# Performance work log

Hardware: AMD Instinct MI355X
Metric: run time of the kernel (lower is better)

Reference implementation:

```python
import jax, jax.numpy as jnp
import numpy as np

HEADS = 16
DIM_HEAD = 64
QUERY_DIM = 1024


def setup_inputs() -> dict:
    key = jax.random.key(0)
    ks = jax.random.split(key, 5)
    B, S, D = 4, 2048, QUERY_DIM
    inner = HEADS * DIM_HEAD
    s = 0.02
    return {
        "x": jax.random.normal(ks[0], (B, S, D), dtype=jnp.float32),
        "Wq": jax.random.normal(ks[1], (D, inner), dtype=jnp.float32) * s,
        "Wk": jax.random.normal(ks[2], (D, inner), dtype=jnp.float32) * s,
        "Wv": jax.random.normal(ks[3], (D, inner), dtype=jnp.float32) * s,
        "Wo": jax.random.normal(ks[4], (inner, D), dtype=jnp.float32) * s,
    }


def reference(x, Wq, Wk, Wv, Wo):
    B, S, D = x.shape
    h, d = HEADS, DIM_HEAD
    scale = d ** (-0.5)
    # projections -> [B, h, S, d]
    q = (x @ Wq).reshape(B, S, h, d).transpose(0, 2, 1, 3)
    k = (x @ Wk).reshape(B, S, h, d).transpose(0, 2, 1, 3)
    v = (x @ Wv).reshape(B, S, h, d).transpose(0, 2, 1, 3)
    # scores [B, h, S, S]
    attn = jnp.einsum("bhqd,bhkd->bhqk", q, k) * scale
    attn = jax.nn.softmax(attn, axis=-1)
    out = jnp.einsum("bhqk,bhkd->bhqd", attn, v)
    out = out.transpose(0, 2, 1, 3).reshape(B, S, h * d)
    return out @ Wo
```

## Files before the change

kernel.cpp:

```cpp
#include <hip/hip_runtime.h>
#include <cstddef>

#define BATCH  4
#define SLEN   2048
#define NHEADS 16
#define DHEAD  64
#define DMODEL 1024

typedef __attribute__((ext_vector_type(8)))  short short8;
typedef __attribute__((ext_vector_type(4)))  float f32x4;
typedef __attribute__((ext_vector_type(16))) float f32x16;

__device__ inline unsigned short f2bf(float f) {
    union { float f; unsigned int u; } v; v.f = f;
    unsigned int r = v.u + 0x7fffu + ((v.u >> 16) & 1u);
    return (unsigned short)(r >> 16);
}

__device__ inline float fast_exp2(float x) {
#if __has_builtin(__builtin_amdgcn_exp2f)
    return __builtin_amdgcn_exp2f(x);
#else
    return __expf(x * 0.69314718f);
#endif
}

__device__ inline void gload_lds16(const unsigned short* g, unsigned short* l) {
    __builtin_amdgcn_global_load_lds(
        (const __attribute__((address_space(1))) void*)g,
        (__attribute__((address_space(3))) void*)l, 16, 0, 0);
}

__global__ __launch_bounds__(256)
void convert_bf16(const float* __restrict__ src, unsigned short* __restrict__ dst, int n8)
{
    const int i = blockIdx.x * 256 + threadIdx.x;
    if (i >= n8) return;
    const float4 a = ((const float4*)src)[2 * i];
    const float4 b = ((const float4*)src)[2 * i + 1];
    short8 o;
    o[0] = (short)f2bf(a.x); o[1] = (short)f2bf(a.y);
    o[2] = (short)f2bf(a.z); o[3] = (short)f2bf(a.w);
    o[4] = (short)f2bf(b.x); o[5] = (short)f2bf(b.y);
    o[6] = (short)f2bf(b.z); o[7] = (short)f2bf(b.w);
    ((short8*)dst)[i] = o;
}

__global__ __launch_bounds__(256)
void wtrans(const float* __restrict__ W0, const float* __restrict__ W1,
            const float* __restrict__ W2, const float* __restrict__ W3,
            unsigned short* __restrict__ T0, unsigned short* __restrict__ T1,
            unsigned short* __restrict__ T2, unsigned short* __restrict__ T3)
{
    const int z = blockIdx.z;
    const float* W = (z == 0) ? W0 : (z == 1) ? W1 : (z == 2) ? W2 : W3;
    unsigned short* Wt = (z == 0) ? T0 : (z == 1) ? T1 : (z == 2) ? T2 : T3;

    __shared__ unsigned short T[64 * 72];
    const int tid = threadIdx.x;
    const int n0 = blockIdx.x * 64, k0 = blockIdx.y * 64;

    #pragma unroll
    for (int it = 0; it < 2; it++) {
        const int t2 = it * 256 + tid;
        const int row = t2 >> 3, col8 = (t2 & 7) * 8;
        const float4 a = *(const float4*)(W + (size_t)(k0 + row) * DMODEL + n0 + col8);
        const float4 b = *(const float4*)(W + (size_t)(k0 + row) * DMODEL + n0 + col8 + 4);
        short8 o;
        o[0] = (short)f2bf(a.x); o[1] = (short)f2bf(a.y);
        o[2] = (short)f2bf(a.z); o[3] = (short)f2bf(a.w);
        o[4] = (short)f2bf(b.x); o[5] = (short)f2bf(b.y);
        o[6] = (short)f2bf(b.z); o[7] = (short)f2bf(b.w);
        *(short8*)&T[row * 72 + col8] = o;
    }
    __syncthreads();
    #pragma unroll
    for (int it = 0; it < 2; it++) {
        const int t2 = it * 256 + tid;
        const int nn = t2 >> 3, k8 = (t2 & 7) * 8;
        short8 v;
        #pragma unroll
        for (int j = 0; j < 8; j++) v[j] = (short)T[(k8 + j) * 72 + nn];
        *(short8*)(Wt + (size_t)(n0 + nn) * DMODEL + k0 + k8) = v;
    }
}

template<int KIND>
__global__ __launch_bounds__(256)
void gemm_bf16(const unsigned short* __restrict__ A,
               const unsigned short* __restrict__ B0,
               const unsigned short* __restrict__ B1,
               const unsigned short* __restrict__ B2,
               void* __restrict__ C0v, void* __restrict__ C1v, void* __restrict__ C2v)
{
    constexpr int N = DMODEL, K = DMODEL;
    __shared__ unsigned short As[128 * 64];
    __shared__ unsigned short Bs[128 * 64];

    const int z = blockIdx.z;
    const unsigned short* Bw = (z == 0) ? B0 : (z == 1) ? B1 : B2;
    void* Cv = (z == 0) ? C0v : (z == 1) ? C1v : C2v;

    const int tid  = threadIdx.x;
    const int lane = tid & 63;
    const int wave = tid >> 6;
    const int c  = lane & 15, qd = lane >> 4;
    const int wr = wave >> 1, wc = wave & 1;
    const int m0 = blockIdx.y * 128, n0 = blockIdx.x * 128;

    const unsigned short* ag[4];
    const unsigned short* bg[4];
    unsigned short* al[4];
    unsigned short* bl[4];
    #pragma unroll
    for (int j = 0; j < 4; j++) {
        const int cid = j * 256 + tid;
        const int row = cid >> 3;
        const int k8  = (cid & 7) ^ (row & 7);
        ag[j] = A  + (size_t)(m0 + row) * K + k8 * 8;
        bg[j] = Bw + (size_t)(n0 + row) * K + k8 * 8;
        al[j] = &As[cid * 8];
        bl[j] = &Bs[cid * 8];
    }

    f32x4 acc[4][4];
    #pragma unroll
    for (int mb = 0; mb < 4; mb++)
        #pragma unroll
        for (int nb = 0; nb < 4; nb++)
            #pragma unroll
            for (int r = 0; r < 4; r++) acc[mb][nb][r] = 0.f;

    for (int k0 = 0; k0 < K; k0 += 64) {
        __syncthreads();
        #pragma unroll
        for (int j = 0; j < 4; j++) {
            gload_lds16(ag[j], al[j]);
            gload_lds16(bg[j], bl[j]);
            ag[j] += 64; bg[j] += 64;
        }
        __syncthreads();

        #pragma unroll
        for (int ks = 0; ks < 2; ks++) {
            const int sw = (ks * 4 + qd) ^ (c & 7);
            short8 af[4], bf[4];
            #pragma unroll
            for (int mb = 0; mb < 4; mb++)
                af[mb] = *(const short8*)&As[((wr * 64 + mb * 16 + c) * 8 + sw) * 8];
            #pragma unroll
            for (int nb = 0; nb < 4; nb++)
                bf[nb] = *(const short8*)&Bs[((wc * 64 + nb * 16 + c) * 8 + sw) * 8];
            #pragma unroll
            for (int mb = 0; mb < 4; mb++)
                #pragma unroll
                for (int nb = 0; nb < 4; nb++)
                    acc[mb][nb] = __builtin_amdgcn_mfma_f32_16x16x32_bf16(
                        af[mb], bf[nb], acc[mb][nb], 0, 0, 0);
        }
    }

    const int mbase = m0 + wr * 64 + qd * 4;
    const int nbase = n0 + wc * 64 + c;
    if (KIND == 1) {
        float* C = (float*)Cv;
        #pragma unroll
        for (int mb = 0; mb < 4; mb++)
            #pragma unroll
            for (int nb = 0; nb < 4; nb++)
                #pragma unroll
                for (int r = 0; r < 4; r++)
                    C[(size_t)(mbase + mb * 16 + r) * N + nbase + nb * 16] = acc[mb][nb][r];
    } else if (z != 2) {
        unsigned short* C = (unsigned short*)Cv;
        const float osc = (z == 0) ? 0.18033688f : 1.0f;
        #pragma unroll
        for (int mb = 0; mb < 4; mb++)
            #pragma unroll
            for (int nb = 0; nb < 4; nb++)
                #pragma unroll
                for (int r = 0; r < 4; r++)
                    C[(size_t)(mbase + mb * 16 + r) * N + nbase + nb * 16] =
                        f2bf(acc[mb][nb][r] * osc);
    } else {
        unsigned short* C = (unsigned short*)Cv;
        const int b = mbase >> 11;
        #pragma unroll
        for (int mb = 0; mb < 4; mb++) {
            const int s = (mbase + mb * 16) & 2047;
            #pragma unroll
            for (int nb = 0; nb < 4; nb++) {
                const int n = nbase + nb * 16;
                const int h = n >> 6, dd = n & 63;
                ushort4 val = make_ushort4(f2bf(acc[mb][nb][0]), f2bf(acc[mb][nb][1]),
                                           f2bf(acc[mb][nb][2]), f2bf(acc[mb][nb][3]));
                *(ushort4*)(C + ((size_t)((b * 16 + h) * 64 + dd)) * SLEN + s) = val;
            }
        }
    }
}

__global__ __launch_bounds__(256, 4)
void attn_mfma6(const unsigned short* __restrict__ qb,
                const unsigned short* __restrict__ kb,
                const unsigned short* __restrict__ vtb,
                unsigned short* __restrict__ O)
{
    __shared__ unsigned short lds[18432];
    unsigned short* Ks = lds;
    unsigned short* Vs = lds + 4096;

    const int tid = threadIdx.x;
    const int w   = tid >> 6, ln = tid & 63;
    const int c5  = ln & 31;
    const int l5i = ln >> 5;

    const int L  = blockIdx.x + (int)gridDim.x * blockIdx.y;
    const int wg = (L & 7) * 128 + (L >> 3);
    const int qt = wg & 15, bh = wg >> 4;
    const int b = bh >> 4, h = bh & 15;
    const size_t bh_base = ((size_t)b * SLEN * NHEADS + h) * 64;
    constexpr int RS = NHEADS * 64;

    const int srow = ln >> 3;
    const int sk8  = (ln & 7) ^ srow;
    const int prow = (srow & 3) | ((w & 1) << 2) | (((srow >> 2) & 1) << 3) | ((w >> 1) << 4);
    const unsigned short* kg0 = kb + bh_base + (size_t)prow * RS + sk8 * 8;
    const unsigned short* kg1 = kg0 + (size_t)32 * RS;
    const unsigned short* vg0 = vtb + ((size_t)bh * 64 + w * 8 + srow) * SLEN + sk8 * 8;
    const unsigned short* vg1 = vg0 + (size_t)32 * SLEN;
    unsigned short* kl0 = &Ks[(w * 64 + ln) * 8];
    unsigned short* kl1 = kl0 + 2048;
    unsigned short* vl0 = &Vs[(w * 64 + ln) * 8];
    unsigned short* vl1 = vl0 + 2048;

    const int qtile = qt * 128 + w * 32;

    short8 qf[4];
    #pragma unroll
    for (int kst = 0; kst < 4; kst++)
        qf[kst] = *(const short8*)(qb + bh_base +
            (size_t)(qtile + c5) * RS + kst * 16 + l5i * 8);

    f32x16 acc[2];
    #pragma unroll
    for (int db = 0; db < 2; db++)
        #pragma unroll
        for (int r = 0; r < 16; r++) acc[db][r] = 0.f;
    float lsum = 0.f;
    const int cl7 = c5 & 7;

    for (int kt = 0; kt < SLEN / 64; kt++) {
        __syncthreads();
        gload_lds16(kg0, kl0); gload_lds16(kg1, kl1);
        gload_lds16(vg0, vl0); gload_lds16(vg1, vl1);
        kg0 += (size_t)64 * RS; kg1 += (size_t)64 * RS; vg0 += 64; vg1 += 64;
        __syncthreads();

        #pragma unroll
        for (int kb32 = 0; kb32 < 2; kb32++) {
            f32x16 sacc;
            #pragma unroll
            for (int r = 0; r < 16; r++) sacc[r] = 0.f;
            __builtin_amdgcn_s_setprio(1);
            #pragma unroll
            for (int kst = 0; kst < 4; kst++) {
                const int slot = (kst * 2 + l5i) ^ cl7;
                short8 kf = *(const short8*)&Ks[((kb32 * 32 + c5) * 8 + slot) * 8];
                sacc = __builtin_amdgcn_mfma_f32_32x32x16_bf16(
                    kf, qf[kst], sacc, 0, 0, 0);
            }
            __builtin_amdgcn_s_setprio(0);

            unsigned pk[8];
            {
                float p[16];
                float s0 = 0.f, s1 = 0.f;
                #pragma unroll
                for (int r = 0; r < 16; r += 2) {
                    p[r]     = fast_exp2(sacc[r]);
                    p[r + 1] = fast_exp2(sacc[r + 1]);
                    s0 += p[r]; s1 += p[r + 1];
                }
                lsum += s0 + s1;
                #pragma unroll
                for (int i = 0; i < 8; i++)
                    pk[i] = __builtin_amdgcn_perm(
                        __float_as_uint(p[2 * i + 1]), __float_as_uint(p[2 * i]),
                        0x07060302u);
            }

            #pragma unroll
            for (int kk = 0; kk < 2; kk++) {
                const int k2 = kb32 * 2 + kk;
                union { unsigned u[4]; short8 s; } t;
                t.u[0] = pk[4 * kk + 0];
                t.u[1] = pk[4 * kk + 1];
                t.u[2] = pk[4 * kk + 2];
                t.u[3] = pk[4 * kk + 3];
                const short8 pf = t.s;
                __builtin_amdgcn_s_setprio(1);
                #pragma unroll
                for (int db = 0; db < 2; db++) {
                    const int slot = (k2 * 2 + l5i) ^ cl7;
                    short8 vf = *(const short8*)&Vs[((db * 32 + c5) * 8 + slot) * 8];
                    acc[db] = __builtin_amdgcn_mfma_f32_32x32x16_bf16(
                        vf, pf, acc[db], 0, 0, 0);
                }
                __builtin_amdgcn_s_setprio(0);
            }
        }
    }

    __syncthreads();
    float l = lsum;
    l += __shfl_xor(l, 32);
    const float inv = 1.001953125f / l;
    unsigned short* E = lds + w * 2304;
    #pragma unroll
    for (int db = 0; db < 2; db++)
        #pragma unroll
        for (int u = 0; u < 4; u++) {
            const int d0 = db * 32 + 8 * u + 4 * l5i;
            const int q  = c5;
            ushort4 val = make_ushort4(
                f2bf(acc[db][4 * u + 0] * inv),
                f2bf(acc[db][4 * u + 1] * inv),
                f2bf(acc[db][4 * u + 2] * inv),
                f2bf(acc[db][4 * u + 3] * inv));
            *(ushort4*)&E[q * 72 + d0] = val;
        }
    __builtin_amdgcn_wave_barrier();
    #pragma unroll
    for (int it = 0; it < 4; it++) {
        const int t2 = it * 64 + ln;
        const int row = t2 >> 3, col8 = (t2 & 7) * 8;
        short8 o = *(const short8*)&E[row * 72 + col8];
        *(short8*)(O + bh_base + (size_t)(qtile + row) * RS + col8) = o;
    }
}

extern "C" void kernel_launch(void* const* d_in, const int* in_sizes, int n_in,
                              void* d_out, int out_size, void* d_ws, size_t ws_size,
                              hipStream_t stream)
{
    const float* x  = (const float*)d_in[0];
    const float* Wq = (const float*)d_in[1];
    const float* Wk = (const float*)d_in[2];
    const float* Wv = (const float*)d_in[3];
    const float* Wo = (const float*)d_in[4];
    float* out = (float*)d_out;

    const size_t per = (size_t)BATCH * SLEN * NHEADS * DHEAD;
    const size_t wsz = (size_t)DMODEL * DMODEL;
    unsigned short* qb  = (unsigned short*)d_ws;
    unsigned short* kb  = qb  + per;
    unsigned short* vtb = kb  + per;
    unsigned short* xb  = vtb + per;
    unsigned short* wtq = xb  + per;
    unsigned short* wtk = wtq + wsz;
    unsigned short* wtv = wtk + wsz;
    unsigned short* wto = wtv + wsz;

    dim3 blk(256);
    convert_bf16<<<dim3((int)(per / 2048)), blk, 0, stream>>>(x, xb, (int)(per / 8));
    wtrans<<<dim3(16, 16, 4), blk, 0, stream>>>(Wq, Wk, Wv, Wo, wtq, wtk, wtv, wto);

    gemm_bf16<0><<<dim3(8, 64, 3), blk, 0, stream>>>(xb, wtq, wtk, wtv, qb, kb, vtb);

    attn_mfma6<<<dim3(SLEN / 128, BATCH * NHEADS), blk, 0, stream>>>(qb, kb, vtb, qb);

    gemm_bf16<1><<<dim3(8, 64, 1), blk, 0, stream>>>(qb, wto, wto, wto, out, out, out);
}
```

Measured before the change: 268.7 us.

## Double-buffer K tiles in LDS and load V fragments directly from global

The attention kernel now double-buffers K tiles in LDS, prefetching the next tile while computing on the current one, which drops one of the two barriers per iteration. V is no longer staged through LDS. Each wave reads its V fragments straight from global memory into registers, which halves LDS use and may raise occupancy. The risk is global-load latency on the V reads, which are not prefetched and come from every wave separately, so L2 traffic rises.

```diff
diff --git a/kernel.cpp b/kernel.cpp
--- a/kernel.cpp
+++ b/kernel.cpp
@@ -201,14 +201,12 @@
 }
 
 __global__ __launch_bounds__(256, 4)
-void attn_mfma6(const unsigned short* __restrict__ qb,
+void attn_mfma8(const unsigned short* __restrict__ qb,
                 const unsigned short* __restrict__ kb,
                 const unsigned short* __restrict__ vtb,
                 unsigned short* __restrict__ O)
 {
-    __shared__ unsigned short lds[18432];
-    unsigned short* Ks = lds;
-    unsigned short* Vs = lds + 4096;
+    __shared__ unsigned short lds[9216];
 
     const int tid = threadIdx.x;
     const int w   = tid >> 6, ln = tid & 63;
@@ -227,12 +225,11 @@
     const int prow = (srow & 3) | ((w & 1) << 2) | (((srow >> 2) & 1) << 3) | ((w >> 1) << 4);
     const unsigned short* kg0 = kb + bh_base + (size_t)prow * RS + sk8 * 8;
     const unsigned short* kg1 = kg0 + (size_t)32 * RS;
-    const unsigned short* vg0 = vtb + ((size_t)bh * 64 + w * 8 + srow) * SLEN + sk8 * 8;
-    const unsigned short* vg1 = vg0 + (size_t)32 * SLEN;
-    unsigned short* kl0 = &Ks[(w * 64 + ln) * 8];
+    unsigned short* kl0 = &lds[(w * 64 + ln) * 8];
     unsigned short* kl1 = kl0 + 2048;
-    unsigned short* vl0 = &Vs[(w * 64 + ln) * 8];
-    unsigned short* vl1 = vl0 + 2048;
+
+    const unsigned short* vr0 = vtb + ((size_t)bh * 64 + c5) * SLEN + l5i * 8;
+    const unsigned short* vr1 = vr0 + (size_t)32 * SLEN;
 
     const int qtile = qt * 128 + w * 32;
 
@@ -250,15 +247,27 @@
     float lsum = 0.f;
     const int cl7 = c5 & 7;
 
+    gload_lds16(kg0, kl0); gload_lds16(kg1, kl1);
+    kg0 += (size_t)64 * RS; kg1 += (size_t)64 * RS;
+    __syncthreads();
+
     for (int kt = 0; kt < SLEN / 64; kt++) {
-        __syncthreads();
-        gload_lds16(kg0, kl0); gload_lds16(kg1, kl1);
-        gload_lds16(vg0, vl0); gload_lds16(vg1, vl1);
-        kg0 += (size_t)64 * RS; kg1 += (size_t)64 * RS; vg0 += 64; vg1 += 64;
-        __syncthreads();
+        const int buf = kt & 1;
+        if (kt < SLEN / 64 - 1) {
+            const int nb = (buf ^ 1) << 12;
+            gload_lds16(kg0, kl0 + nb);
+            gload_lds16(kg1, kl1 + nb);
+            kg0 += (size_t)64 * RS; kg1 += (size_t)64 * RS;
+        }
+        const unsigned short* Kb = &lds[buf << 12];
 
         #pragma unroll
         for (int kb32 = 0; kb32 < 2; kb32++) {
+            const short8 vf00 = *(const short8*)(vr0 + kb32 * 32);
+            const short8 vf01 = *(const short8*)(vr1 + kb32 * 32);
+            const short8 vf10 = *(const short8*)(vr0 + kb32 * 32 + 16);
+            const short8 vf11 = *(const short8*)(vr1 + kb32 * 32 + 16);
+
             f32x16 sacc;
             #pragma unroll
             for (int r = 0; r < 16; r++) sacc[r] = 0.f;
@@ -266,7 +275,7 @@
             #pragma unroll
             for (int kst = 0; kst < 4; kst++) {
                 const int slot = (kst * 2 + l5i) ^ cl7;
-                short8 kf = *(const short8*)&Ks[((kb32 * 32 + c5) * 8 + slot) * 8];
+                short8 kf = *(const short8*)&Kb[((kb32 * 32 + c5) * 8 + slot) * 8];
                 sacc = __builtin_amdgcn_mfma_f32_32x32x16_bf16(
                     kf, qf[kst], sacc, 0, 0, 0);
             }
@@ -292,7 +301,6 @@
 
             #pragma unroll
             for (int kk = 0; kk < 2; kk++) {
-                const int k2 = kb32 * 2 + kk;
                 union { unsigned u[4]; short8 s; } t;
                 t.u[0] = pk[4 * kk + 0];
                 t.u[1] = pk[4 * kk + 1];
@@ -300,19 +308,17 @@
                 t.u[3] = pk[4 * kk + 3];
                 const short8 pf = t.s;
                 __builtin_amdgcn_s_setprio(1);
-                #pragma unroll
-                for (int db = 0; db < 2; db++) {
-                    const int slot = (k2 * 2 + l5i) ^ cl7;
-                    short8 vf = *(const short8*)&Vs[((db * 32 + c5) * 8 + slot) * 8];
-                    acc[db] = __builtin_amdgcn_mfma_f32_32x32x16_bf16(
-                        vf, pf, acc[db], 0, 0, 0);
-                }
+                acc[0] = __builtin_amdgcn_mfma_f32_32x32x16_bf16(
+                    kk == 0 ? vf00 : vf10, pf, acc[0], 0, 0, 0);
+                acc[1] = __builtin_amdgcn_mfma_f32_32x32x16_bf16(
+                    kk == 0 ? vf01 : vf11, pf, acc[1], 0, 0, 0);
                 __builtin_amdgcn_s_setprio(0);
             }
         }
-    }
-
-    __syncthreads();
+        __syncthreads();
+        vr0 += 64; vr1 += 64;
+    }
+
     float l = lsum;
     l += __shfl_xor(l, 32);
     const float inv = 1.001953125f / l;
@@ -368,7 +374,7 @@
 
     gemm_bf16<0><<<dim3(8, 64, 3), blk, 0, stream>>>(xb, wtq, wtk, wtv, qb, kb, vtb);
 
-    attn_mfma6<<<dim3(SLEN / 128, BATCH * NHEADS), blk, 0, stream>>>(qb, kb, vtb, qb);
+    attn_mfma8<<<dim3(SLEN / 128, BATCH * NHEADS), blk, 0, stream>>>(qb, kb, vtb, qb);
 
     gemm_bf16<1><<<dim3(8, 64, 1), blk, 0, stream>>>(qb, wto, wto, wto, out, out, out);
 }
```

Result: slower. 321.9 us (+19.8%).

## Double-buffer K/V tiles in attention and merge prep kernels into one launch

Applied to the files above, without the earlier changes.

The attention kernel now prefetches the next K/V tile into a second LDS buffer while computing on the current one, replacing the load-then-sync pattern with a single barrier per iteration. This is meant to hide global-to-LDS load latency behind MFMA work. The x conversion and weight transpose kernels are fused into a single launch to save one kernel launch. LDS per block rises to 32 KB, which may constrain occupancy.

```diff
diff --git a/kernel.cpp b/kernel.cpp
--- a/kernel.cpp
+++ b/kernel.cpp
@@ -32,33 +32,34 @@
 }
 
 __global__ __launch_bounds__(256)
-void convert_bf16(const float* __restrict__ src, unsigned short* __restrict__ dst, int n8)
+void prep(const float* __restrict__ x, unsigned short* __restrict__ xb,
+          const float* __restrict__ W0, const float* __restrict__ W1,
+          const float* __restrict__ W2, const float* __restrict__ W3,
+          unsigned short* __restrict__ T0, unsigned short* __restrict__ T1,
+          unsigned short* __restrict__ T2, unsigned short* __restrict__ T3)
 {
-    const int i = blockIdx.x * 256 + threadIdx.x;
-    if (i >= n8) return;
-    const float4 a = ((const float4*)src)[2 * i];
-    const float4 b = ((const float4*)src)[2 * i + 1];
-    short8 o;
-    o[0] = (short)f2bf(a.x); o[1] = (short)f2bf(a.y);
-    o[2] = (short)f2bf(a.z); o[3] = (short)f2bf(a.w);
-    o[4] = (short)f2bf(b.x); o[5] = (short)f2bf(b.y);
-    o[6] = (short)f2bf(b.z); o[7] = (short)f2bf(b.w);
-    ((short8*)dst)[i] = o;
-}
-
-__global__ __launch_bounds__(256)
-void wtrans(const float* __restrict__ W0, const float* __restrict__ W1,
-            const float* __restrict__ W2, const float* __restrict__ W3,
-            unsigned short* __restrict__ T0, unsigned short* __restrict__ T1,
-            unsigned short* __restrict__ T2, unsigned short* __restrict__ T3)
-{
-    const int z = blockIdx.z;
+    __shared__ unsigned short T[64 * 72];
+    const int bid = blockIdx.x;
+    const int tid = threadIdx.x;
+
+    if (bid < 4096) {
+        const int i = bid * 256 + tid;
+        const float4 a = ((const float4*)x)[2 * i];
+        const float4 b = ((const float4*)x)[2 * i + 1];
+        short8 o;
+        o[0] = (short)f2bf(a.x); o[1] = (short)f2bf(a.y);
+        o[2] = (short)f2bf(a.z); o[3] = (short)f2bf(a.w);
+        o[4] = (short)f2bf(b.x); o[5] = (short)f2bf(b.y);
+        o[6] = (short)f2bf(b.z); o[7] = (short)f2bf(b.w);
+        ((short8*)xb)[i] = o;
+        return;
+    }
+
+    const int idx = bid - 4096;
+    const int z = idx >> 8;
     const float* W = (z == 0) ? W0 : (z == 1) ? W1 : (z == 2) ? W2 : W3;
     unsigned short* Wt = (z == 0) ? T0 : (z == 1) ? T1 : (z == 2) ? T2 : T3;
-
-    __shared__ unsigned short T[64 * 72];
-    const int tid = threadIdx.x;
-    const int n0 = blockIdx.x * 64, k0 = blockIdx.y * 64;
+    const int n0 = (idx & 15) * 64, k0 = ((idx >> 4) & 15) * 64;
 
     #pragma unroll
     for (int it = 0; it < 2; it++) {
@@ -201,14 +202,14 @@
 }
 
 __global__ __launch_bounds__(256, 4)
-void attn_mfma6(const unsigned short* __restrict__ qb,
+void attn_mfma9(const unsigned short* __restrict__ qb,
                 const unsigned short* __restrict__ kb,
                 const unsigned short* __restrict__ vtb,
                 unsigned short* __restrict__ O)
 {
-    __shared__ unsigned short lds[18432];
+    __shared__ unsigned short lds[16384];
     unsigned short* Ks = lds;
-    unsigned short* Vs = lds + 4096;
+    unsigned short* Vs = lds + 8192;
 
     const int tid = threadIdx.x;
     const int w   = tid >> 6, ln = tid & 63;
@@ -250,12 +251,21 @@
     float lsum = 0.f;
     const int cl7 = c5 & 7;
 
+    gload_lds16(kg0, kl0); gload_lds16(kg1, kl1);
+    gload_lds16(vg0, vl0); gload_lds16(vg1, vl1);
+    kg0 += (size_t)64 * RS; kg1 += (size_t)64 * RS; vg0 += 64; vg1 += 64;
+    __syncthreads();
+
     for (int kt = 0; kt < SLEN / 64; kt++) {
-        __syncthreads();
-        gload_lds16(kg0, kl0); gload_lds16(kg1, kl1);
-        gload_lds16(vg0, vl0); gload_lds16(vg1, vl1);
-        kg0 += (size_t)64 * RS; kg1 += (size_t)64 * RS; vg0 += 64; vg1 += 64;
-        __syncthreads();
+        const int buf = kt & 1;
+        if (kt < SLEN / 64 - 1) {
+            const int nb = (buf ^ 1) * 4096;
+            gload_lds16(kg0, kl0 + nb); gload_lds16(kg1, kl1 + nb);
+            gload_lds16(vg0, vl0 + nb); gload_lds16(vg1, vl1 + nb);
+            kg0 += (size_t)64 * RS; kg1 += (size_t)64 * RS; vg0 += 64; vg1 += 64;
+        }
+        const unsigned short* Kb = Ks + buf * 4096;
+        const unsigned short* Vb = Vs + buf * 4096;
 
         #pragma unroll
         for (int kb32 = 0; kb32 < 2; kb32++) {
@@ -266,7 +276,7 @@
             #pragma unroll
             for (int kst = 0; kst < 4; kst++) {
                 const int slot = (kst * 2 + l5i) ^ cl7;
-                short8 kf = *(const short8*)&Ks[((kb32 * 32 + c5) * 8 + slot) * 8];
+                short8 kf = *(const short8*)&Kb[((kb32 * 32 + c5) * 8 + slot) * 8];
                 sacc = __builtin_amdgcn_mfma_f32_32x32x16_bf16(
                     kf, qf[kst], sacc, 0, 0, 0);
             }
@@ -303,16 +313,16 @@
                 #pragma unroll
                 for (int db = 0; db < 2; db++) {
                     const int slot = (k2 * 2 + l5i) ^ cl7;
-                    short8 vf = *(const short8*)&Vs[((db * 32 + c5) * 8 + slot) * 8];
+                    short8 vf = *(const short8*)&Vb[((db * 32 + c5) * 8 + slot) * 8];
                     acc[db] = __builtin_amdgcn_mfma_f32_32x32x16_bf16(
                         vf, pf, acc[db], 0, 0, 0);
                 }
                 __builtin_amdgcn_s_setprio(0);
             }
         }
-    }
-
-    __syncthreads();
+        __syncthreads();
+    }
+
     float l = lsum;
     l += __shfl_xor(l, 32);
     const float inv = 1.001953125f / l;
@@ -363,12 +373,12 @@
     unsigned short* wto = wtv + wsz;
 
     dim3 blk(256);
-    convert_bf16<<<dim3((int)(per / 2048)), blk, 0, stream>>>(x, xb, (int)(per / 8));
-    wtrans<<<dim3(16, 16, 4), blk, 0, stream>>>(Wq, Wk, Wv, Wo, wtq, wtk, wtv, wto);
+    prep<<<dim3(4096 + 1024), blk, 0, stream>>>(x, xb, Wq, Wk, Wv, Wo,
+                                                wtq, wtk, wtv, wto);
 
     gemm_bf16<0><<<dim3(8, 64, 3), blk, 0, stream>>>(xb, wtq, wtk, wtv, qb, kb, vtb);
 
-    attn_mfma6<<<dim3(SLEN / 128, BATCH * NHEADS), blk, 0, stream>>>(qb, kb, vtb, qb);
+    attn_mfma9<<<dim3(SLEN / 128, BATCH * NHEADS), blk, 0, stream>>>(qb, kb, vtb, qb);
 
     gemm_bf16<1><<<dim3(8, 64, 1), blk, 0, stream>>>(qb, wto, wto, wto, out, out, out);
 }
```

New measurement: 264.0 us. No clear change (-1.7%).
